# Optimization experiments

Hardware: AMD Instinct MI355X
Metric: run time of the kernel (lower is better)

Reference implementation:

```python
import jax, jax.numpy as jnp
import numpy as np

T, D, H, E = 8192, 1024, 4096, 8

def setup_inputs() -> dict:
    key = jax.random.key(0)
    k1, k2, k3, k4 = jax.random.split(key, 4)
    x = jax.random.normal(k1, (T, D), dtype=jnp.float32)
    Wg = jax.random.normal(k2, (E, D), dtype=jnp.float32) * (1.0 / np.sqrt(D))
    W1 = jax.random.normal(k3, (E, D, H), dtype=jnp.float32) * (1.0 / np.sqrt(D))
    W2 = jax.random.normal(k4, (E, H, D), dtype=jnp.float32) * (1.0 / np.sqrt(H))
    return {"x": x, "Wg": Wg, "W1": W1, "W2": W2, "top_k": 2}


def reference(x, Wg, W1, W2, top_k):
    # Router: logits -> softmax over experts -> top-k -> renormalize
    router_logits = x @ Wg.T                                   # [T, E]
    rw = jax.nn.softmax(router_logits.astype(jnp.float32), axis=1)
    w, sel = jax.lax.top_k(rw, top_k)                          # [T, k]
    w = w / jnp.sum(w, axis=-1, keepdims=True)
    w = w.astype(x.dtype)

    n_exp, hid = W1.shape[0], W1.shape[2]
    # Expert FFN up-projection: grouped GEMM expressed as per-expert dense
    # matmuls (fixed small expert loop), selecting rows by routing mask.
    h = jnp.zeros((x.shape[0], top_k, hid), dtype=x.dtype)     # [T, k, H]
    for e in range(n_exp):
        he = x @ W1[e]                                         # [T, H]
        m = sel == e                                           # [T, k]
        h = jnp.where(m[..., None], he[:, None, :], h)
    h = jax.nn.gelu(h, approximate=False)

    # Down-projection + gated combine. Gating is applied before the second
    # linear (equivalent to scatter-with-gates after, since GEMM is linear).
    y = jnp.zeros_like(x)                                      # [T, D]
    for e in range(n_exp):
        m = (sel == e).astype(x.dtype) * w                     # [T, k]
        hm = jnp.einsum('tk,tkh->th', m, h)                    # gated combine per expert
        y = y + hm @ W2[e]
    return (y, router_logits)
```

## Files before the change

kernel.cpp:

```cpp
#include <hip/hip_runtime.h>
#include <math.h>


#define T_TOK 8192
#define DDIM 1024
#define HDIM 4096
#define NEXP 8
#define BM 128
#define BN 128
#define BK 32
#define R_MAX (T_TOK * 2)
#define R_PAD (R_MAX + NEXP * BM)
#define ROWTILES ((R_MAX / BM) + NEXP)

typedef unsigned short u16;
typedef unsigned int u32;
typedef __attribute__((ext_vector_type(4))) float f32x4;
typedef __attribute__((ext_vector_type(8))) short bf16x8;

__device__ __forceinline__ u16 f2bf(float f) {
  union { float f; u32 u; } v; v.f = f;
  u32 r = v.u + 0x7fffu + ((v.u >> 16) & 1u);
  return (u16)(r >> 16);
}
__device__ __forceinline__ float bf2f(u16 h) {
  union { u32 u; float f; } v; v.u = ((u32)h) << 16; return v.f;
}
__device__ __forceinline__ void gll16(const void* g, void* l) {
  __builtin_amdgcn_global_load_lds(
      (const __attribute__((address_space(1))) u32*)g,
      (__attribute__((address_space(3))) u32*)l, 16, 0, 0);
}

__global__ __launch_bounds__(256) void k_router(const float* __restrict__ x,
                                                const float* __restrict__ Wg,
                                                float* __restrict__ logits,
                                                int* __restrict__ sel,
                                                float* __restrict__ wts) {
  __shared__ float wg[NEXP * DDIM];
  const int t = threadIdx.x;
  for (int i = t; i < NEXP * DDIM; i += 256) wg[i] = Wg[i];
  __syncthreads();
  const int wave = t >> 6, lane = t & 63;
  const int tok = blockIdx.x * 4 + wave;
  const float* xr = x + (size_t)tok * DDIM;
  float acc[NEXP];
#pragma unroll
  for (int e = 0; e < NEXP; ++e) acc[e] = 0.f;
  for (int c = 0; c < DDIM / 64; ++c) {
    const float xv = xr[c * 64 + lane];
#pragma unroll
    for (int e = 0; e < NEXP; ++e) acc[e] += xv * wg[e * DDIM + c * 64 + lane];
  }
#pragma unroll
  for (int e = 0; e < NEXP; ++e) {
    float v = acc[e];
    for (int off = 32; off; off >>= 1) v += __shfl_xor(v, off, 64);
    acc[e] = v;
  }
  if (lane < NEXP) logits[(size_t)tok * NEXP + lane] = acc[lane];
  if (lane == 0) {
    int i1 = 0; float m1 = acc[0];
#pragma unroll
    for (int e = 1; e < NEXP; ++e) if (acc[e] > m1) { m1 = acc[e]; i1 = e; }
    int i2 = -1; float m2 = -INFINITY;
#pragma unroll
    for (int e = 0; e < NEXP; ++e) if (e != i1 && acc[e] > m2) { m2 = acc[e]; i2 = e; }
    const float ex = expf(m2 - m1);
    const float w1 = 1.f / (1.f + ex);
    sel[tok * 2 + 0] = i1; sel[tok * 2 + 1] = i2;
    wts[tok * 2 + 0] = w1; wts[tok * 2 + 1] = ex * w1;
  }
}

__global__ __launch_bounds__(256) void k_count(const int* __restrict__ sel, int* __restrict__ cnt) {
  const int t = blockIdx.x * 256 + threadIdx.x;
  const int lane = threadIdx.x & 63;
  for (int k = 0; k < 2; ++k) {
    const int s = sel[t * 2 + k];
#pragma unroll
    for (int e = 0; e < NEXP; ++e) {
      const unsigned long long m = __ballot(s == e);
      if (m && lane == __builtin_ctzll(m)) atomicAdd(&cnt[e], __popcll(m));
    }
  }
}

__global__ void k_scan(const int* __restrict__ cnt, int* __restrict__ poff) {
  if (threadIdx.x == 0 && blockIdx.x == 0) {
    int run = 0;
    for (int e = 0; e < NEXP; ++e) { poff[e] = run; run += ((cnt[e] + BM - 1) / BM) * BM; }
    poff[NEXP] = run;
  }
}

__global__ __launch_bounds__(256) void k_scatter(const int* __restrict__ sel,
                                                 const float* __restrict__ wts,
                                                 const int* __restrict__ poff,
                                                 int* __restrict__ cursor,
                                                 int* __restrict__ rows,
                                                 float* __restrict__ gw,
                                                 int* __restrict__ posof) {
  const int t = blockIdx.x * 256 + threadIdx.x;
  const int lane = threadIdx.x & 63;
  for (int k = 0; k < 2; ++k) {
    const int s = sel[t * 2 + k];
    const float w = wts[t * 2 + k];
#pragma unroll
    for (int e = 0; e < NEXP; ++e) {
      const unsigned long long m = __ballot(s == e);
      if (!m) continue;
      const int leader = __builtin_ctzll(m);
      int base = 0;
      if (lane == leader) base = atomicAdd(&cursor[e], (int)__popcll(m));
      base = __shfl(base, leader, 64);
      if (s == e) {
        const int pos = base + (int)__popcll(m & ((1ull << lane) - 1ull));
        const int g = poff[e] + pos;
        rows[g] = t; gw[g] = w; posof[t * 2 + k] = g;
      }
    }
  }
}

__global__ __launch_bounds__(256) void k_splitx(const float* __restrict__ x,
                                                u16* __restrict__ xhi, u16* __restrict__ xlo,
                                                int wlo) {
  const size_t i = (size_t)blockIdx.x * 256 + threadIdx.x;
  const float4 v = ((const float4*)x)[i];
  float vv[4] = {v.x, v.y, v.z, v.w};
  u16 h[4], l[4];
#pragma unroll
  for (int j = 0; j < 4; ++j) { h[j] = f2bf(vv[j]); l[j] = f2bf(vv[j] - bf2f(h[j])); }
  ((ushort4*)xhi)[i] = make_ushort4(h[0], h[1], h[2], h[3]);
  if (wlo) ((ushort4*)xlo)[i] = make_ushort4(l[0], l[1], l[2], l[3]);
}

__global__ __launch_bounds__(256) void k_tsplit(const float* __restrict__ in,
                                                u16* __restrict__ ohi, u16* __restrict__ olo,
                                                int Rr, int Cc, int wlo) {
  __shared__ float tile[64][65];
  const int tilesC = Cc / 64;
  const int per = (Rr / 64) * tilesC;
  const int e = blockIdx.x / per, rem = blockIdx.x % per;
  const int rt = rem / tilesC, ct = rem % tilesC;
  const float* bin = in + ((size_t)e * Rr + rt * 64) * Cc + ct * 64;
  const int r0 = threadIdx.x >> 6, c = threadIdx.x & 63;
#pragma unroll
  for (int i = 0; i < 16; ++i) tile[i * 4 + r0][c] = bin[(size_t)(i * 4 + r0) * Cc + c];
  __syncthreads();
  u16* bhi = ohi + ((size_t)e * Cc + ct * 64) * Rr + rt * 64;
  u16* blo = wlo ? olo + ((size_t)e * Cc + ct * 64) * Rr + rt * 64 : nullptr;
#pragma unroll
  for (int i = 0; i < 16; ++i) {
    const int orow = i * 4 + r0;
    const float v = tile[c][orow];
    const u16 h = f2bf(v);
    bhi[(size_t)orow * Rr + c] = h;
    if (wlo) blo[(size_t)orow * Rr + c] = f2bf(v - bf2f(h));
  }
}

template <bool IS_UP, bool ALO, bool BLO, bool WLO>
__global__ __launch_bounds__(256, 2) void k_gemm(
    const u16* __restrict__ Ahi, const u16* __restrict__ Alo,
    const u16* __restrict__ Bhi, const u16* __restrict__ Blo,
    const int* __restrict__ poff, const int* __restrict__ cnt,
    const int* __restrict__ rows, const float* __restrict__ gw,
    u16* __restrict__ OHi, u16* __restrict__ OLo, float* __restrict__ OF) {
  constexpr int KD = IS_UP ? DDIM : HDIM;
  constexpr int ND = IS_UP ? HDIM : DDIM;
  constexpr int NT = ND / BN;
  const int rt = blockIdx.x / NT, ct = blockIdx.x % NT;
  const int r0 = rt * BM;
  if (r0 >= poff[NEXP]) return;
  int e = 0;
#pragma unroll
  for (int i = 1; i < NEXP; ++i) if (r0 >= poff[i]) e = i;
  const int lim = poff[e] + cnt[e];
  const int n0 = ct * BN;

  __shared__ __align__(16) u16 sA[2][BM * BK];
  __shared__ __align__(16) u16 sB[2][BN * BK];
  __shared__ float s_gw[BM];

  const int t = threadIdx.x;
  const int wave = t >> 6, lane = t & 63;

  const char *aHi[2], *aLo[2], *bHi[2], *bLo[2];
#pragma unroll
  for (int i = 0; i < 2; ++i) {
    const int m = i * 64 + (t >> 2);
    size_t arow;
    if constexpr (IS_UP) {
      const int gr = r0 + m;
      const int tok = (gr < lim) ? rows[gr] : 0;
      arow = (size_t)tok * DDIM;
    } else {
      arow = (size_t)(r0 + m) * HDIM;
    }
    aHi[i] = (const char*)Ahi + arow * 2 + (t & 3) * 16;
    if constexpr (ALO) aLo[i] = (const char*)Alo + arow * 2 + (t & 3) * 16;
    const size_t brow = ((size_t)e * ND + n0 + m) * KD;
    bHi[i] = (const char*)Bhi + brow * 2 + (t & 3) * 16;
    if constexpr (BLO) bLo[i] = (const char*)Blo + brow * 2 + (t & 3) * 16;
  }
  if constexpr (IS_UP) {
    if (t < BM) { const int gr = r0 + t; s_gw[t] = (gr < lim) ? gw[gr] : 0.f; }
  }

  f32x4 acc[4][4];
#pragma unroll
  for (int a = 0; a < 4; ++a)
#pragma unroll
    for (int b = 0; b < 4; ++b) acc[a][b] = {0.f, 0.f, 0.f, 0.f};

  const int wm0 = (wave >> 1) * 64, wn0 = (wave & 1) * 64;
  const int c16 = lane & 15, grp = lane >> 4;

  for (int kt = 0; kt < KD / BK; ++kt) {
    __syncthreads();
    const size_t kb = (size_t)kt * (BK * 2);
#pragma unroll
    for (int i = 0; i < 2; ++i) {
      gll16(aHi[i] + kb, (char*)&sA[0][0] + i * 4096 + wave * 1024);
      gll16(bHi[i] + kb, (char*)&sB[0][0] + i * 4096 + wave * 1024);
      if constexpr (ALO) gll16(aLo[i] + kb, (char*)&sA[1][0] + i * 4096 + wave * 1024);
      if constexpr (BLO) gll16(bLo[i] + kb, (char*)&sB[1][0] + i * 4096 + wave * 1024);
    }
    __syncthreads();

    bf16x8 fa[4], fb[4], fal[4], fbl[4];
#pragma unroll
    for (int mf = 0; mf < 4; ++mf) {
      const int off = (wm0 + mf * 16 + c16) * BK + grp * 8;
      fa[mf] = *(const bf16x8*)&sA[0][off];
      if constexpr (ALO) fal[mf] = *(const bf16x8*)&sA[1][off];
    }
#pragma unroll
    for (int nf = 0; nf < 4; ++nf) {
      const int off = (wn0 + nf * 16 + c16) * BK + grp * 8;
      fb[nf] = *(const bf16x8*)&sB[0][off];
      if constexpr (BLO) fbl[nf] = *(const bf16x8*)&sB[1][off];
    }
#pragma unroll
    for (int mf = 0; mf < 4; ++mf)
#pragma unroll
      for (int nf = 0; nf < 4; ++nf) {
        acc[mf][nf] = __builtin_amdgcn_mfma_f32_16x16x32_bf16(fa[mf], fb[nf], acc[mf][nf], 0, 0, 0);
        if constexpr (BLO)
          acc[mf][nf] = __builtin_amdgcn_mfma_f32_16x16x32_bf16(fa[mf], fbl[nf], acc[mf][nf], 0, 0, 0);
        if constexpr (ALO)
          acc[mf][nf] = __builtin_amdgcn_mfma_f32_16x16x32_bf16(fal[mf], fb[nf], acc[mf][nf], 0, 0, 0);
      }
  }

#pragma unroll
  for (int mf = 0; mf < 4; ++mf) {
#pragma unroll
    for (int q = 0; q < 4; ++q) {
      const int r = wm0 + mf * 16 + grp * 4 + q;
      const int gr = r0 + r;
      if (gr < lim) {
        if constexpr (IS_UP) {
          const float g = s_gw[r];
#pragma unroll
          for (int nf = 0; nf < 4; ++nf) {
            const int gc = n0 + wn0 + nf * 16 + c16;
            const float v = acc[mf][nf][q];
            const float hg = 0.5f * v * (1.f + erff(v * 0.7071067811865476f)) * g;
            const u16 h = f2bf(hg);
            OHi[(size_t)gr * HDIM + gc] = h;
            if constexpr (WLO) OLo[(size_t)gr * HDIM + gc] = f2bf(hg - bf2f(h));
          }
        } else {
#pragma unroll
          for (int nf = 0; nf < 4; ++nf) {
            const int gc = n0 + wn0 + nf * 16 + c16;
            OF[(size_t)gr * DDIM + gc] = acc[mf][nf][q];
          }
        }
      }
    }
  }
}

__global__ __launch_bounds__(256) void k_combine(const float* __restrict__ yd,
                                                 const int* __restrict__ posof,
                                                 float* __restrict__ y) {
  const size_t i = (size_t)blockIdx.x * 256 + threadIdx.x;
  const int t = (int)(i >> 8), c = (int)(i & 255);
  const int p0 = posof[t * 2], p1 = posof[t * 2 + 1];
  const float4 a = ((const float4*)yd)[(size_t)p0 * 256 + c];
  const float4 b = ((const float4*)yd)[(size_t)p1 * 256 + c];
  float4 r; r.x = a.x + b.x; r.y = a.y + b.y; r.z = a.z + b.z; r.w = a.w + b.w;
  ((float4*)y)[i] = r;
}

extern "C" void kernel_launch(void* const* d_in, const int* in_sizes, int n_in,
                              void* d_out, int out_size, void* d_ws, size_t ws_size,
                              hipStream_t stream) {
  const float* x  = (const float*)d_in[0];
  const float* Wg = (const float*)d_in[1];
  const float* W1 = (const float*)d_in[2];
  const float* W2 = (const float*)d_in[3];
  float* y = (float*)d_out;
  float* logits = y + (size_t)T_TOK * DDIM;

  char* ws = (char*)d_ws;
  int* cnt    = (int*)(ws + 0);
  int* cursor = (int*)(ws + 64);
  int* poff   = (int*)(ws + 128);
  size_t o = 256;
  int*   sel   = (int*)(ws + o);   o += (size_t)R_MAX * 4;
  float* wts   = (float*)(ws + o); o += (size_t)R_MAX * 4;
  int*   posof = (int*)(ws + o);   o += (size_t)R_MAX * 4;
  int*   rows  = (int*)(ws + o);   o += (size_t)R_PAD * 4;
  float* gwp   = (float*)(ws + o); o += (size_t)R_PAD * 4;
  o = (o + 255) & ~(size_t)255;
  const size_t S_XP = (size_t)T_TOK * DDIM * 2;
  const size_t S_WP = (size_t)NEXP * HDIM * DDIM * 2;
  const size_t S_HP = (size_t)R_PAD * HDIM * 2;
  const size_t S_YD = (size_t)R_PAD * DDIM * 4;
  u16* xhi  = (u16*)(ws + o); o += S_XP;
  u16* w1hi = (u16*)(ws + o); o += S_WP;
  u16* w2hi = (u16*)(ws + o); o += S_WP;
  u16* hhi  = (u16*)(ws + o); o += S_HP;
  float* yd = (float*)(ws + o); o += S_YD;
  u16* xlo  = (u16*)(ws + o); o += S_XP;
  u16* w1lo = (u16*)(ws + o); o += S_WP;
  u16* w2lo = (u16*)(ws + o); o += S_WP;
  const size_t need1 = o;
  u16* hlo  = (u16*)(ws + o); o += S_HP;
  const size_t need2 = o;
  const int lvl = (ws_size >= need2) ? 2 : (ws_size >= need1) ? 1 : 0;

  hipMemsetAsync(d_ws, 0, 256, stream);
  k_router<<<T_TOK / 4, 256, 0, stream>>>(x, Wg, logits, sel, wts);
  k_count<<<T_TOK / 256, 256, 0, stream>>>(sel, cnt);
  k_scan<<<1, 64, 0, stream>>>(cnt, poff);
  k_scatter<<<T_TOK / 256, 256, 0, stream>>>(sel, wts, poff, cursor, rows, gwp, posof);
  k_splitx<<<(T_TOK * DDIM / 4) / 256, 256, 0, stream>>>(x, xhi, xlo, lvl >= 1);
  const int tgrid = NEXP * (DDIM / 64) * (HDIM / 64);
  k_tsplit<<<tgrid, 256, 0, stream>>>(W1, w1hi, w1lo, DDIM, HDIM, lvl >= 1);
  k_tsplit<<<tgrid, 256, 0, stream>>>(W2, w2hi, w2lo, HDIM, DDIM, lvl >= 1);

  const int upGrid = ROWTILES * (HDIM / BN);
  const int dnGrid = ROWTILES * (DDIM / BN);
  if (lvl == 2) {
    k_gemm<true,  true,  true,  true ><<<upGrid, 256, 0, stream>>>(xhi, xlo, w1hi, w1lo, poff, cnt, rows, gwp, hhi, hlo, nullptr);
    k_gemm<false, true,  true,  false><<<dnGrid, 256, 0, stream>>>(hhi, hlo, w2hi, w2lo, poff, cnt, rows, gwp, nullptr, nullptr, yd);
  } else if (lvl == 1) {
    k_gemm<true,  true,  true,  false><<<upGrid, 256, 0, stream>>>(xhi, xlo, w1hi, w1lo, poff, cnt, rows, gwp, hhi, nullptr, nullptr);
    k_gemm<false, false, true,  false><<<dnGrid, 256, 0, stream>>>(hhi, nullptr, w2hi, w2lo, poff, cnt, rows, gwp, nullptr, nullptr, yd);
  } else {
    k_gemm<true,  false, false, false><<<upGrid, 256, 0, stream>>>(xhi, nullptr, w1hi, nullptr, poff, cnt, rows, gwp, hhi, nullptr, nullptr);
    k_gemm<false, false, false, false><<<dnGrid, 256, 0, stream>>>(hhi, nullptr, w2hi, nullptr, poff, cnt, rows, gwp, nullptr, nullptr, yd);
  }
  k_combine<<<(T_TOK * DDIM / 4) / 256, 256, 0, stream>>>(yd, posof, y);
}
```

Baseline: 1.189 ms.

## Fuse W2 transpose-split into up-GEMM launch, swizzle LDS, remap block order

The W2 transpose/bf16-split work now runs as extra workgroups inside the up-projection GEMM launch, dropping a separate kernel and letting it overlap with GEMM tiles. The GEMM gains an XOR swizzle on the LDS layout to cut bank conflicts on fragment reads. It also remaps block IDs (stride-8 interleave), and allocates shared memory sized to the hi/lo planes actually used, which can raise occupancy for lower precision levels. The transpose writes become ushort4 vectorized stores. The risks are added LDS pressure from the union buffer in the fused kernel and load imbalance between the two kinds of workgroup.

```diff
diff --git a/kernel.cpp b/kernel.cpp
--- a/kernel.cpp
+++ b/kernel.cpp
@@ -136,33 +136,47 @@
   if (wlo) ((ushort4*)xlo)[i] = make_ushort4(l[0], l[1], l[2], l[3]);
 }
 
+__device__ __forceinline__ void tsplit_body(int bid, char* smemRaw,
+                                            const float* __restrict__ in,
+                                            u16* __restrict__ ohi, u16* __restrict__ olo,
+                                            int Rr, int Cc, int wlo) {
+  float (*tile)[65] = (float (*)[65])smemRaw;
+  const int tilesC = Cc >> 6;
+  const int per = (Rr >> 6) * tilesC;
+  const int e = bid / per, rem = bid % per;
+  const int rt = rem / tilesC, ct = rem % tilesC;
+  const float* bin = in + ((size_t)e * Rr + rt * 64) * Cc + ct * 64;
+  const int t = threadIdx.x;
+  const int r0 = t >> 6, c = t & 63;
+#pragma unroll
+  for (int i = 0; i < 16; ++i) tile[i * 4 + r0][c] = bin[(size_t)(i * 4 + r0) * Cc + c];
+  __syncthreads();
+  u16* bhi = ohi + ((size_t)e * Cc + ct * 64) * Rr + rt * 64;
+  u16* blo = olo + ((size_t)e * Cc + ct * 64) * Rr + rt * 64;
+#pragma unroll
+  for (int j = 0; j < 4; ++j) {
+    const int idx = t + j * 256;
+    const int orow = idx >> 4, ch = idx & 15;
+    u16 h[4], l[4];
+#pragma unroll
+    for (int q = 0; q < 4; ++q) {
+      const float v = tile[ch * 4 + q][orow];
+      h[q] = f2bf(v); l[q] = f2bf(v - bf2f(h[q]));
+    }
+    *(ushort4*)&bhi[(size_t)orow * Rr + ch * 4] = make_ushort4(h[0], h[1], h[2], h[3]);
+    if (wlo) *(ushort4*)&blo[(size_t)orow * Rr + ch * 4] = make_ushort4(l[0], l[1], l[2], l[3]);
+  }
+}
+
 __global__ __launch_bounds__(256) void k_tsplit(const float* __restrict__ in,
                                                 u16* __restrict__ ohi, u16* __restrict__ olo,
                                                 int Rr, int Cc, int wlo) {
-  __shared__ float tile[64][65];
-  const int tilesC = Cc / 64;
-  const int per = (Rr / 64) * tilesC;
-  const int e = blockIdx.x / per, rem = blockIdx.x % per;
-  const int rt = rem / tilesC, ct = rem % tilesC;
-  const float* bin = in + ((size_t)e * Rr + rt * 64) * Cc + ct * 64;
-  const int r0 = threadIdx.x >> 6, c = threadIdx.x & 63;
-#pragma unroll
-  for (int i = 0; i < 16; ++i) tile[i * 4 + r0][c] = bin[(size_t)(i * 4 + r0) * Cc + c];
-  __syncthreads();
-  u16* bhi = ohi + ((size_t)e * Cc + ct * 64) * Rr + rt * 64;
-  u16* blo = wlo ? olo + ((size_t)e * Cc + ct * 64) * Rr + rt * 64 : nullptr;
-#pragma unroll
-  for (int i = 0; i < 16; ++i) {
-    const int orow = i * 4 + r0;
-    const float v = tile[c][orow];
-    const u16 h = f2bf(v);
-    bhi[(size_t)orow * Rr + c] = h;
-    if (wlo) blo[(size_t)orow * Rr + c] = f2bf(v - bf2f(h));
-  }
+  __shared__ char smem[64 * 65 * 4];
+  tsplit_body(blockIdx.x, smem, in, ohi, olo, Rr, Cc, wlo);
 }
 
 template <bool IS_UP, bool ALO, bool BLO, bool WLO>
-__global__ __launch_bounds__(256, 2) void k_gemm(
+__device__ __forceinline__ void gemm_body(int bid0, char* smemRaw,
     const u16* __restrict__ Ahi, const u16* __restrict__ Alo,
     const u16* __restrict__ Bhi, const u16* __restrict__ Blo,
     const int* __restrict__ poff, const int* __restrict__ cnt,
@@ -171,7 +185,11 @@
   constexpr int KD = IS_UP ? DDIM : HDIM;
   constexpr int ND = IS_UP ? HDIM : DDIM;
   constexpr int NT = ND / BN;
-  const int rt = blockIdx.x / NT, ct = blockIdx.x % NT;
+  constexpr int APL = ALO ? 2 : 1;
+  constexpr int BPL = BLO ? 2 : 1;
+  constexpr int NWG = ROWTILES * NT;
+  const int bid = (bid0 & 7) * (NWG >> 3) + (bid0 >> 3);
+  const int rt = bid / NT, ct = bid % NT;
   const int r0 = rt * BM;
   if (r0 >= poff[NEXP]) return;
   int e = 0;
@@ -180,12 +198,13 @@
   const int lim = poff[e] + cnt[e];
   const int n0 = ct * BN;
 
-  __shared__ __align__(16) u16 sA[2][BM * BK];
-  __shared__ __align__(16) u16 sB[2][BN * BK];
-  __shared__ float s_gw[BM];
+  u16* sA = (u16*)smemRaw;
+  u16* sB = (u16*)(smemRaw + APL * BM * BK * 2);
+  float* s_gw = (float*)(smemRaw + (APL + BPL) * BM * BK * 2);
 
   const int t = threadIdx.x;
   const int wave = t >> 6, lane = t & 63;
+  const int gsw = (((t & 3) ^ ((t >> 3) & 3)) << 4);
 
   const char *aHi[2], *aLo[2], *bHi[2], *bLo[2];
 #pragma unroll
@@ -199,11 +218,11 @@
     } else {
       arow = (size_t)(r0 + m) * HDIM;
     }
-    aHi[i] = (const char*)Ahi + arow * 2 + (t & 3) * 16;
-    if constexpr (ALO) aLo[i] = (const char*)Alo + arow * 2 + (t & 3) * 16;
+    aHi[i] = (const char*)Ahi + arow * 2 + gsw;
+    if constexpr (ALO) aLo[i] = (const char*)Alo + arow * 2 + gsw;
     const size_t brow = ((size_t)e * ND + n0 + m) * KD;
-    bHi[i] = (const char*)Bhi + brow * 2 + (t & 3) * 16;
-    if constexpr (BLO) bLo[i] = (const char*)Blo + brow * 2 + (t & 3) * 16;
+    bHi[i] = (const char*)Bhi + brow * 2 + gsw;
+    if constexpr (BLO) bLo[i] = (const char*)Blo + brow * 2 + gsw;
   }
   if constexpr (IS_UP) {
     if (t < BM) { const int gr = r0 + t; s_gw[t] = (gr < lim) ? gw[gr] : 0.f; }
@@ -217,31 +236,32 @@
 
   const int wm0 = (wave >> 1) * 64, wn0 = (wave & 1) * 64;
   const int c16 = lane & 15, grp = lane >> 4;
+  const int gsr = (grp ^ ((c16 >> 1) & 3)) << 3;
 
   for (int kt = 0; kt < KD / BK; ++kt) {
     __syncthreads();
     const size_t kb = (size_t)kt * (BK * 2);
 #pragma unroll
     for (int i = 0; i < 2; ++i) {
-      gll16(aHi[i] + kb, (char*)&sA[0][0] + i * 4096 + wave * 1024);
-      gll16(bHi[i] + kb, (char*)&sB[0][0] + i * 4096 + wave * 1024);
-      if constexpr (ALO) gll16(aLo[i] + kb, (char*)&sA[1][0] + i * 4096 + wave * 1024);
-      if constexpr (BLO) gll16(bLo[i] + kb, (char*)&sB[1][0] + i * 4096 + wave * 1024);
+      gll16(aHi[i] + kb, (char*)sA + i * 4096 + wave * 1024);
+      gll16(bHi[i] + kb, (char*)sB + i * 4096 + wave * 1024);
+      if constexpr (ALO) gll16(aLo[i] + kb, (char*)sA + 8192 + i * 4096 + wave * 1024);
+      if constexpr (BLO) gll16(bLo[i] + kb, (char*)sB + 8192 + i * 4096 + wave * 1024);
     }
     __syncthreads();
 
     bf16x8 fa[4], fb[4], fal[4], fbl[4];
 #pragma unroll
     for (int mf = 0; mf < 4; ++mf) {
-      const int off = (wm0 + mf * 16 + c16) * BK + grp * 8;
-      fa[mf] = *(const bf16x8*)&sA[0][off];
-      if constexpr (ALO) fal[mf] = *(const bf16x8*)&sA[1][off];
+      const int off = (wm0 + mf * 16 + c16) * BK + gsr;
+      fa[mf] = *(const bf16x8*)&sA[off];
+      if constexpr (ALO) fal[mf] = *(const bf16x8*)&sA[BM * BK + off];
     }
 #pragma unroll
     for (int nf = 0; nf < 4; ++nf) {
-      const int off = (wn0 + nf * 16 + c16) * BK + grp * 8;
-      fb[nf] = *(const bf16x8*)&sB[0][off];
-      if constexpr (BLO) fbl[nf] = *(const bf16x8*)&sB[1][off];
+      const int off = (wn0 + nf * 16 + c16) * BK + gsr;
+      fb[nf] = *(const bf16x8*)&sB[off];
+      if constexpr (BLO) fbl[nf] = *(const bf16x8*)&sB[BN * BK + off];
     }
 #pragma unroll
     for (int mf = 0; mf < 4; ++mf)
@@ -283,6 +303,37 @@
       }
     }
   }
+}
+
+template <bool ALO, bool BLO>
+__global__ __launch_bounds__(256, 2) void k_gemm_dn(
+    const u16* __restrict__ Ahi, const u16* __restrict__ Alo,
+    const u16* __restrict__ Bhi, const u16* __restrict__ Blo,
+    const int* __restrict__ poff, const int* __restrict__ cnt,
+    float* __restrict__ OF) {
+  constexpr int SZ = ((ALO ? 2 : 1) + (BLO ? 2 : 1)) * BM * BK * 2 + 16;
+  __shared__ __align__(16) char smem[SZ];
+  gemm_body<false, ALO, BLO, false>(blockIdx.x, smem, Ahi, Alo, Bhi, Blo,
+                                    poff, cnt, nullptr, nullptr, nullptr, nullptr, OF);
+}
+
+#define UPGRID (ROWTILES * (HDIM / BN))
+template <bool ALO, bool BLO, bool WLO>
+__global__ __launch_bounds__(256, 2) void k_up_fused(
+    const u16* __restrict__ Ahi, const u16* __restrict__ Alo,
+    const u16* __restrict__ Bhi, const u16* __restrict__ Blo,
+    const int* __restrict__ poff, const int* __restrict__ cnt,
+    const int* __restrict__ rows, const float* __restrict__ gw,
+    u16* __restrict__ OHi, u16* __restrict__ OLo,
+    const float* __restrict__ W2, u16* __restrict__ w2hi, u16* __restrict__ w2lo, int wlo) {
+  constexpr int GSZ = ((ALO ? 2 : 1) + (BLO ? 2 : 1)) * BM * BK * 2 + BM * 4;
+  constexpr int SZ = GSZ > (64 * 65 * 4) ? GSZ : (64 * 65 * 4);
+  __shared__ __align__(16) char smem[SZ];
+  if (blockIdx.x < UPGRID)
+    gemm_body<true, ALO, BLO, WLO>(blockIdx.x, smem, Ahi, Alo, Bhi, Blo,
+                                   poff, cnt, rows, gw, OHi, OLo, nullptr);
+  else
+    tsplit_body(blockIdx.x - UPGRID, smem, W2, w2hi, w2lo, HDIM, DDIM, wlo);
 }
 
 __global__ __launch_bounds__(256) void k_combine(const float* __restrict__ yd,
@@ -343,19 +394,21 @@
   k_splitx<<<(T_TOK * DDIM / 4) / 256, 256, 0, stream>>>(x, xhi, xlo, lvl >= 1);
   const int tgrid = NEXP * (DDIM / 64) * (HDIM / 64);
   k_tsplit<<<tgrid, 256, 0, stream>>>(W1, w1hi, w1lo, DDIM, HDIM, lvl >= 1);
-  k_tsplit<<<tgrid, 256, 0, stream>>>(W2, w2hi, w2lo, HDIM, DDIM, lvl >= 1);
-
-  const int upGrid = ROWTILES * (HDIM / BN);
+
+  const int fusedGrid = UPGRID + tgrid;
   const int dnGrid = ROWTILES * (DDIM / BN);
   if (lvl == 2) {
-    k_gemm<true,  true,  true,  true ><<<upGrid, 256, 0, stream>>>(xhi, xlo, w1hi, w1lo, poff, cnt, rows, gwp, hhi, hlo, nullptr);
-    k_gemm<false, true,  true,  false><<<dnGrid, 256, 0, stream>>>(hhi, hlo, w2hi, w2lo, poff, cnt, rows, gwp, nullptr, nullptr, yd);
+    k_up_fused<true, true, true><<<fusedGrid, 256, 0, stream>>>(
+        xhi, xlo, w1hi, w1lo, poff, cnt, rows, gwp, hhi, hlo, W2, w2hi, w2lo, 1);
+    k_gemm_dn<true, true><<<dnGrid, 256, 0, stream>>>(hhi, hlo, w2hi, w2lo, poff, cnt, yd);
   } else if (lvl == 1) {
-    k_gemm<true,  true,  true,  false><<<upGrid, 256, 0, stream>>>(xhi, xlo, w1hi, w1lo, poff, cnt, rows, gwp, hhi, nullptr, nullptr);
-    k_gemm<false, false, true,  false><<<dnGrid, 256, 0, stream>>>(hhi, nullptr, w2hi, w2lo, poff, cnt, rows, gwp, nullptr, nullptr, yd);
+    k_up_fused<true, true, false><<<fusedGrid, 256, 0, stream>>>(
+        xhi, xlo, w1hi, w1lo, poff, cnt, rows, gwp, hhi, nullptr, W2, w2hi, w2lo, 1);
+    k_gemm_dn<false, true><<<dnGrid, 256, 0, stream>>>(hhi, nullptr, w2hi, w2lo, poff, cnt, yd);
   } else {
-    k_gemm<true,  false, false, false><<<upGrid, 256, 0, stream>>>(xhi, nullptr, w1hi, nullptr, poff, cnt, rows, gwp, hhi, nullptr, nullptr);
-    k_gemm<false, false, false, false><<<dnGrid, 256, 0, stream>>>(hhi, nullptr, w2hi, nullptr, poff, cnt, rows, gwp, nullptr, nullptr, yd);
+    k_up_fused<false, false, false><<<fusedGrid, 256, 0, stream>>>(
+        xhi, nullptr, w1hi, nullptr, poff, cnt, rows, gwp, hhi, nullptr, W2, w2hi, w2lo, 0);
+    k_gemm_dn<false, false><<<dnGrid, 256, 0, stream>>>(hhi, nullptr, w2hi, nullptr, poff, cnt, yd);
   }
   k_combine<<<(T_TOK * DDIM / 4) / 256, 256, 0, stream>>>(yd, posof, y);
 }
```

After: 1.165 ms. 2.0% less time.
